# Optimization experiments

Measured on AMD Instinct MI355X. Metric: run time of the kernel, lower is better.

The kernel has to match this reference:

```python
import jax, jax.numpy as jnp
import numpy as np

B, S, PLM, G = 8, 2048, 768, 256
N_WM, E_WM = 50000, 800000
N_F, E_F = B * S, 131072
K = 4


def _gnn(h, src, dst, Ws, bs, n_nodes):
    # simple GCN-style message passing: aggregate neighbor features via
    # gather (h[src]) + scatter-add (segment_sum), then linear + relu.
    for W, b in zip(Ws, bs):
        m = jax.ops.segment_sum(h[src], dst, num_segments=n_nodes)  # [n, g]
        h = jax.nn.relu((h + m) @ W + b)
    return h


def setup_inputs() -> dict:
    key = jax.random.key(0)
    ks = jax.random.split(key, 16)
    std = 0.02
    inp = {
        "text_embeddings": jax.random.normal(ks[0], (B, S, PLM), jnp.float32),
        "wm_x": jax.random.normal(ks[1], (N_WM, G), jnp.float32),
        "wm_edge_index": jax.random.randint(ks[2], (2, E_WM), 0, N_WM),
        "token2nodepos": jax.random.randint(ks[3], (B * S, K), 0, N_WM),
        "fstm_node_ids": jax.random.randint(ks[4], (N_F,), 0, N_F),
        "fstm_edge_index": jax.random.randint(ks[5], (2, E_F), 0, N_F),
        # extra_emb: nn.Embedding(2, G, padding_idx=0) -> row 0 is zeros
        "extra_emb": jax.random.normal(ks[6], (2, G), jnp.float32).at[0].set(0.0) * std,
        "wm_W1": jax.random.normal(ks[7], (G, G), jnp.float32) * std,
        "wm_b1": jnp.zeros((G,), jnp.float32),
        "wm_W2": jax.random.normal(ks[8], (G, G), jnp.float32) * std,
        "wm_b2": jnp.zeros((G,), jnp.float32),
        "fstm_W1": jax.random.normal(ks[9], (G, G), jnp.float32) * std,
        "fstm_b1": jnp.zeros((G,), jnp.float32),
        "fstm_W2": jax.random.normal(ks[10], (G, G), jnp.float32) * std,
        "fstm_b2": jnp.zeros((G,), jnp.float32),
        "fc1_W": jax.random.normal(ks[11], (G + PLM, G), jnp.float32) * std,
        "fc1_b": jnp.zeros((G,), jnp.float32),
        "fc3_W": jax.random.normal(ks[12], (PLM + 2 * G, PLM), jnp.float32) * std,
        "fc3_b": jnp.zeros((PLM,), jnp.float32),
    }
    return inp


def reference(text_embeddings, wm_x, wm_edge_index, token2nodepos, fstm_node_ids,
              fstm_edge_index, extra_emb, wm_W1, wm_b1, wm_W2, wm_b2,
              fstm_W1, fstm_b1, fstm_W2, fstm_b2, fc1_W, fc1_b, fc3_W, fc3_b):
    # ====== WM ======
    graph_embeddings = _gnn(wm_x, wm_edge_index[0], wm_edge_index[1],
                            (wm_W1, wm_W2), (wm_b1, wm_b2), N_WM)  # [N_WM, G]
    table = jnp.concatenate([extra_emb, graph_embeddings], axis=0)  # [N_WM+2, G]
    # per-token gather-sum over K concept slots (original python loop, vectorized)
    tmp = jnp.sum(table[token2nodepos + 2], axis=1)  # [B*S, G]
    text_flat = text_embeddings.reshape(B * S, PLM)
    graph_text_embed = jnp.concatenate([tmp, text_flat], axis=-1) @ fc1_W + fc1_b  # [B*S, G]
    # ====== FSTM ======
    x = graph_text_embed[fstm_node_ids]  # [B*S, G]
    temporal = _gnn(x, fstm_edge_index[0], fstm_edge_index[1],
                    (fstm_W1, fstm_W2), (fstm_b1, fstm_b2), N_F)
    temporal = temporal.reshape(B, S, G)
    # ====== Final ======
    final_vec = jnp.concatenate(
        [text_embeddings, tmp.reshape(B, S, G), temporal], axis=-1)
    logits = final_vec @ fc3_W + fc3_b  # [B, S, PLM]
    return logits
```

## Files before the change

kernel.cpp:

```cpp
#include <hip/hip_runtime.h>

#define Bsz 8
#define Ssz 2048
#define PLM 768
#define Gd  256
#define N_WM 50000
#define E_WM 800000
#define N_F  16384
#define E_F  131072
#define Kc   4

typedef unsigned short ushort_t;
typedef short short8 __attribute__((ext_vector_type(8)));
typedef float f32x4 __attribute__((ext_vector_type(4)));

__device__ __forceinline__ ushort_t f2bf(float f) {
    union { float f; unsigned int u; } v; v.f = f;
    unsigned int r = (v.u + 0x7fffu + ((v.u >> 16) & 1u)) >> 16;
    return (ushort_t)r;
}
__device__ __forceinline__ float bf2f(ushort_t b) {
    union { unsigned int u; float f; } v; v.u = ((unsigned int)b) << 16;
    return v.f;
}
__device__ __forceinline__ float4 bf4f(ushort4 u) {
    return make_float4(bf2f(u.x), bf2f(u.y), bf2f(u.z), bf2f(u.w));
}

__device__ __forceinline__ void gl2lds16(const ushort_t* g, ushort_t* l) {
    __builtin_amdgcn_global_load_lds(
        (const __attribute__((address_space(1))) unsigned int*)g,
        (__attribute__((address_space(3))) unsigned int*)l, 16, 0, 0);
}

__device__ __forceinline__ void cvt4(const float* __restrict__ in,
                                     ushort_t* __restrict__ out, int i, int n4) {
    if (i < n4) {
        float4 v = ((const float4*)in)[i];
        ushort4 u;
        u.x = f2bf(v.x); u.y = f2bf(v.y); u.z = f2bf(v.z); u.w = f2bf(v.w);
        ((ushort4*)out)[i] = u;
    }
}

__device__ __forceinline__ void wtx_tile(const float* __restrict__ W,
                                         ushort_t* __restrict__ Wt,
                                         int K, int N, int tile,
                                         ushort_t (*sm)[65]) {
    int kt = K >> 6;
    int k0 = (tile % kt) << 6;
    int n0 = (tile / kt) << 6;
    int t = threadIdx.x;
    int tr = t >> 6, tc = t & 63;
#pragma unroll
    for (int p = 0; p < 16; ++p) {
        int k = p * 4 + tr;
        sm[k][tc] = f2bf(W[(size_t)(k0 + k) * N + n0 + tc]);
    }
    __syncthreads();
#pragma unroll
    for (int p = 0; p < 16; ++p) {
        int n = p * 4 + tr;
        Wt[(size_t)(n0 + n) * K + k0 + tc] = sm[tc][n];
    }
}

__global__ void conv_all(const float* __restrict__ wm_x, const float* __restrict__ text,
                         const float* __restrict__ extra,
                         const float* __restrict__ W1, const float* __restrict__ W2,
                         const float* __restrict__ W3, const float* __restrict__ W4,
                         const float* __restrict__ W5, const float* __restrict__ W6,
                         ushort_t* __restrict__ Xb, ushort_t* __restrict__ Tx,
                         ushort_t* __restrict__ Exb,
                         ushort_t* __restrict__ T1, ushort_t* __restrict__ T2,
                         ushort_t* __restrict__ T3, ushort_t* __restrict__ T4,
                         ushort_t* __restrict__ T5, ushort_t* __restrict__ T6) {
    __shared__ ushort_t sm[64][65];
    int b = blockIdx.x, t = threadIdx.x;
    if (b < 12500) { cvt4(wm_x, Xb, b * 256 + t, 3200000); return; }
    b -= 12500;
    if (b < 12288) { cvt4(text, Tx, b * 256 + t, 3145728); return; }
    b -= 12288;
    if (b < 1) { cvt4(extra, Exb, t, 128); return; }
    b -= 1;
    if (b < 16) { wtx_tile(W1, T1, 256, 256, b, sm); return; }
    b -= 16;
    if (b < 16) { wtx_tile(W2, T2, 256, 256, b, sm); return; }
    b -= 16;
    if (b < 16) { wtx_tile(W3, T3, 256, 256, b, sm); return; }
    b -= 16;
    if (b < 16) { wtx_tile(W4, T4, 256, 256, b, sm); return; }
    b -= 16;
    if (b < 64) { wtx_tile(W5, T5, 1024, 256, b, sm); return; }
    b -= 64;
    wtx_tile(W6, T6, 1280, 768, b, sm);
}

#define WM_P 512
#define WM_CH 1563
#define WM_SHIFT 8
#define FS_P 128
#define FS_CH 1024
#define FS_SHIFT 6

__global__ __launch_bounds__(256) void csr_p1(const int* __restrict__ wm_dst,
                                              const int* __restrict__ f_dst,
                                              int* __restrict__ Cwm,
                                              int* __restrict__ Cfs) {
    __shared__ int hist[256];
    int b = blockIdx.x, t = threadIdx.x;
    hist[t] = 0; __syncthreads();
    if (b < WM_P) {
        int e0 = b * WM_CH, e1 = e0 + WM_CH; if (e1 > E_WM) e1 = E_WM;
        for (int e = e0 + t; e < e1; e += 256)
            atomicAdd(&hist[wm_dst[e] >> WM_SHIFT], 1);
        __syncthreads();
        Cwm[b * 256 + t] = hist[t];
    } else {
        int p = b - WM_P;
        int e0 = p * FS_CH, e1 = e0 + FS_CH;
        for (int e = e0 + t; e < e1; e += 256)
            atomicAdd(&hist[f_dst[e] >> FS_SHIFT], 1);
        __syncthreads();
        Cfs[p * 256 + t] = hist[t];
    }
}

__global__ __launch_bounds__(256) void csr_p2a(int* __restrict__ Cwm, int* __restrict__ BTwm,
                                               int* __restrict__ Cfs, int* __restrict__ BTfs) {
    __shared__ int sm[256];
    int b = blockIdx.x, t = threadIdx.x;
    int* C; int* BT; int P; int bk;
    if (b < 256) { C = Cwm; BT = BTwm; P = WM_P; bk = b; }
    else         { C = Cfs; BT = BTfs; P = FS_P; bk = b - 256; }
    int half = P >> 1;
    int v0 = 0, v1 = 0;
    if (t < half) { v0 = C[(2 * t) * 256 + bk]; v1 = C[(2 * t + 1) * 256 + bk]; }
    int s = v0 + v1;
    sm[t] = s; __syncthreads();
#pragma unroll
    for (int st = 1; st < 256; st <<= 1) {
        int x = (t >= st) ? sm[t - st] : 0;
        __syncthreads();
        sm[t] += x;
        __syncthreads();
    }
    int ex = sm[t] - s;
    if (t < half) {
        C[(2 * t) * 256 + bk] = ex;
        C[(2 * t + 1) * 256 + bk] = ex + v0;
    }
    if (t == 255) BT[bk] = sm[255];
}

__global__ __launch_bounds__(256) void csr_p2b(const int* __restrict__ BTwm,
                                               int* __restrict__ BSwm,
                                               const int* __restrict__ BTfs,
                                               int* __restrict__ BSfs) {
    __shared__ int sm[256];
    int t = threadIdx.x;
    const int* BT = blockIdx.x ? BTfs : BTwm;
    int* BS = blockIdx.x ? BSfs : BSwm;
    int E = blockIdx.x ? E_F : E_WM;
    int v = BT[t];
    sm[t] = v; __syncthreads();
#pragma unroll
    for (int st = 1; st < 256; st <<= 1) {
        int x = (t >= st) ? sm[t - st] : 0;
        __syncthreads();
        sm[t] += x;
        __syncthreads();
    }
    BS[t] = sm[t] - v;
    if (t == 255) BS[256] = E;
}

__global__ __launch_bounds__(256) void csr_p3(const int* __restrict__ wm_src,
                                              const int* __restrict__ wm_dst,
                                              const int* __restrict__ Cwm,
                                              const int* __restrict__ BSwm,
                                              int2* __restrict__ SEwm,
                                              const int* __restrict__ f_src,
                                              const int* __restrict__ f_dst,
                                              const int* __restrict__ Cfs,
                                              const int* __restrict__ BSfs,
                                              int2* __restrict__ SEfs) {
    __shared__ int cur[256];
    int b = blockIdx.x, t = threadIdx.x;
    if (b < WM_P) {
        cur[t] = Cwm[b * 256 + t] + BSwm[t];
        __syncthreads();
        int e0 = b * WM_CH, e1 = e0 + WM_CH; if (e1 > E_WM) e1 = E_WM;
        for (int e = e0 + t; e < e1; e += 256) {
            int d = wm_dst[e], s = wm_src[e];
            int pos = atomicAdd(&cur[d >> WM_SHIFT], 1);
            SEwm[pos] = make_int2(s, d);
        }
    } else {
        int p = b - WM_P;
        cur[t] = Cfs[p * 256 + t] + BSfs[t];
        __syncthreads();
        int e0 = p * FS_CH, e1 = e0 + FS_CH;
        for (int e = e0 + t; e < e1; e += 256) {
            int d = f_dst[e], s = f_src[e];
            int pos = atomicAdd(&cur[d >> FS_SHIFT], 1);
            SEfs[pos] = make_int2(s, d);
        }
    }
}

__global__ __launch_bounds__(256) void csr_p4(const int2* __restrict__ SEwm,
                                              const int* __restrict__ BSwm,
                                              int* __restrict__ wm_off,
                                              int* __restrict__ wm_bkt,
                                              const int2* __restrict__ SEfs,
                                              const int* __restrict__ BSfs,
                                              int* __restrict__ fs_off,
                                              int* __restrict__ fs_bkt) {
    __shared__ int cnt[256];
    __shared__ int sm[256];
    int ob = blockIdx.x, t = threadIdx.x;
    const int2* SE; const int* BS; int* off; int* bkt;
    int b, nb0, n, E, bw;
    if (ob < 256) { SE = SEwm; BS = BSwm; off = wm_off; bkt = wm_bkt;
                    b = ob; nb0 = b << WM_SHIFT; n = N_WM; E = E_WM; bw = 256; }
    else          { SE = SEfs; BS = BSfs; off = fs_off; bkt = fs_bkt;
                    b = ob - 256; nb0 = b << FS_SHIFT; n = N_F; E = E_F; bw = 64; }
    int e0 = BS[b], e1 = BS[b + 1];
    cnt[t] = 0; __syncthreads();
    for (int e = e0 + t; e < e1; e += 256)
        atomicAdd(&cnt[SE[e].y - nb0], 1);
    __syncthreads();
    int v = cnt[t];
    sm[t] = v; __syncthreads();
#pragma unroll
    for (int st = 1; st < 256; st <<= 1) {
        int x = (t >= st) ? sm[t - st] : 0;
        __syncthreads();
        sm[t] += x;
        __syncthreads();
    }
    int ex = sm[t] - v;
    if (t < bw && nb0 + t < n) off[nb0 + t] = e0 + ex;
    if (b == 0 && t == 0) off[n] = E;
    __syncthreads();
    cnt[t] = e0 + ex;
    __syncthreads();
    for (int e = e0 + t; e < e1; e += 256) {
        int2 sd = SE[e];
        int pos = atomicAdd(&cnt[sd.y - nb0], 1);
        bkt[pos] = sd.x;
    }
}

__global__ void aggregate_kernel(const ushort_t* __restrict__ h,
                                 const int* __restrict__ off,
                                 const int* __restrict__ bucket,
                                 ushort_t* __restrict__ hm, int n) {
    int i = blockIdx.x * 4 + (threadIdx.x >> 6);
    if (i >= n) return;
    int lane = threadIdx.x & 63;
    int s0 = off[i], s1 = off[i + 1];
    const ushort4* hp = (const ushort4*)h;
    float4 acc = bf4f(hp[(size_t)i * 64 + lane]);
    int j = s0;
    for (; j + 16 <= s1; j += 16) {
        int bb[16];
#pragma unroll
        for (int q = 0; q < 16; ++q) bb[q] = bucket[j + q];
        ushort4 rr[16];
#pragma unroll
        for (int q = 0; q < 16; ++q) rr[q] = hp[(size_t)bb[q] * 64 + lane];
#pragma unroll
        for (int q = 0; q < 16; ++q) {
            float4 v = bf4f(rr[q]);
            acc.x += v.x; acc.y += v.y; acc.z += v.z; acc.w += v.w;
        }
    }
    for (; j + 4 <= s1; j += 4) {
        int bb[4];
#pragma unroll
        for (int q = 0; q < 4; ++q) bb[q] = bucket[j + q];
        ushort4 rr[4];
#pragma unroll
        for (int q = 0; q < 4; ++q) rr[q] = hp[(size_t)bb[q] * 64 + lane];
#pragma unroll
        for (int q = 0; q < 4; ++q) {
            float4 v = bf4f(rr[q]);
            acc.x += v.x; acc.y += v.y; acc.z += v.z; acc.w += v.w;
        }
    }
    for (; j < s1; ++j) {
        float4 v = bf4f(hp[(size_t)bucket[j] * 64 + lane]);
        acc.x += v.x; acc.y += v.y; acc.z += v.z; acc.w += v.w;
    }
    ushort4 u;
    u.x = f2bf(acc.x); u.y = f2bf(acc.y); u.z = f2bf(acc.z); u.w = f2bf(acc.w);
    ((ushort4*)hm)[(size_t)i * 64 + lane] = u;
}

__global__ void tmp_kernel(const ushort_t* __restrict__ gemb,
                           const ushort_t* __restrict__ extra,
                           const int* __restrict__ t2np,
                           ushort_t* __restrict__ D) {
    int i = blockIdx.x * 4 + (threadIdx.x >> 6);
    int lane = threadIdx.x & 63;
    float4 s = make_float4(0.f, 0.f, 0.f, 0.f);
#pragma unroll
    for (int k = 0; k < Kc; ++k) {
        int idx = t2np[i * Kc + k] + 2;
        const ushort4* row = (idx < 2) ? (const ushort4*)(extra + (size_t)idx * Gd)
                                       : (const ushort4*)(gemb + (size_t)(idx - 2) * Gd);
        float4 v = bf4f(row[lane]);
        s.x += v.x; s.y += v.y; s.z += v.z; s.w += v.w;
    }
    ushort4 u;
    u.x = f2bf(s.x); u.y = f2bf(s.y); u.z = f2bf(s.z); u.w = f2bf(s.w);
    ((ushort4*)D)[(size_t)i * 64 + lane] = u;
}

__global__ void gather_kernel(const ushort_t* __restrict__ Ein,
                              const int* __restrict__ ids,
                              ushort_t* __restrict__ F) {
    int i = blockIdx.x * 4 + (threadIdx.x >> 6);
    int lane = threadIdx.x & 63;
    ((ushort4*)F)[(size_t)i * 64 + lane] =
        ((const ushort4*)Ein)[(size_t)ids[i] * 64 + lane];
}

#define TBK 64
#define GBM 64
#define GBN 128

__device__ __forceinline__ void xcd_swizzle(int& bx, int& by) {
    int gx = gridDim.x;
    int nwg = gx * gridDim.y;
    int orig = by * gx + bx;
    int q = nwg >> 3, r = nwg & 7;
    int xcd = orig & 7, loc = orig >> 3;
    int wg = (xcd < r ? xcd * (q + 1) : r * (q + 1) + (xcd - r) * q) + loc;
    bx = wg % gx;
    by = wg / gx;
}

template <int MODE, int OUTBF, int BM, int BN>
__global__ __launch_bounds__(256) void mfma_gemm(
    const ushort_t* __restrict__ p0, const ushort_t* __restrict__ p1,
    const ushort_t* __restrict__ p2, const ushort_t* __restrict__ Wt,
    const float* __restrict__ bias, void* __restrict__ Cv,
    int M, int N, int K, int relu) {
    constexpr int MR = BM / 32;
    constexpr int NR = BN / 32;
    constexpr int A_IT = (BM * TBK) / 2048;
    constexpr int B_IT = (BN * TBK) / 2048;
    __shared__ ushort_t As[BM * TBK];
    __shared__ ushort_t Bs[BN * TBK];

    int tid  = threadIdx.x;
    int lane = tid & 63;
    int wave = tid >> 6;
    int wm = (wave >> 1) * (BM / 2), wn = (wave & 1) * (BN / 2);
    int bx = blockIdx.x, by = blockIdx.y;
    xcd_swizzle(bx, by);
    int row0 = by * BM, col0 = bx * BN;
    int l15 = lane & 15, l4 = lane >> 4;

    f32x4 acc[MR][NR];
#pragma unroll
    for (int i = 0; i < MR; ++i)
#pragma unroll
        for (int j = 0; j < NR; ++j)
            acc[i][j] = (f32x4){0.f, 0.f, 0.f, 0.f};

    for (int k0 = 0; k0 < K; k0 += TBK) {
#pragma unroll
        for (int it = 0; it < A_IT; ++it) {
            int eb = it * 2048 + wave * 512;
            int le = eb + lane * 8;
            int r  = le >> 6;
            int kl = (le ^ ((r & 7) << 3)) & 63;
            int grow = row0 + r; if (grow > M - 1) grow = M - 1;
            int gk = k0 + kl;
            const ushort_t* gp;
            if (MODE == 0)
                gp = p0 + (size_t)grow * K + gk;
            else if (MODE == 2)
                gp = (gk < 256) ? p0 + (size_t)grow * 256 + gk
                                : p1 + (size_t)grow * 768 + (gk - 256);
            else
                gp = (gk < 768) ? p0 + (size_t)grow * 768 + gk
                   : (gk < 1024) ? p1 + (size_t)grow * 256 + (gk - 768)
                                 : p2 + (size_t)grow * 256 + (gk - 1024);
            gl2lds16(gp, &As[eb]);
        }
#pragma unroll
        for (int it = 0; it < B_IT; ++it) {
            int eb = it * 2048 + wave * 512;
            int le = eb + lane * 8;
            int nl = le >> 6;
            int kl = (le ^ ((nl & 7) << 3)) & 63;
            const ushort_t* gp = Wt + (size_t)(col0 + nl) * K + k0 + kl;
            gl2lds16(gp, &Bs[eb]);
        }
        __syncthreads();

#pragma unroll
        for (int ks = 0; ks < TBK; ks += 32) {
            short8 af[MR], bfr[NR];
#pragma unroll
            for (int mi = 0; mi < MR; ++mi) {
                int row = wm + mi * 16 + l15;
                int col = (ks + l4 * 8) ^ ((row & 7) << 3);
                af[mi] = *(const short8*)&As[row * TBK + col];
            }
#pragma unroll
            for (int ni = 0; ni < NR; ++ni) {
                int row = wn + ni * 16 + l15;
                int col = (ks + l4 * 8) ^ ((row & 7) << 3);
                bfr[ni] = *(const short8*)&Bs[row * TBK + col];
            }
#pragma unroll
            for (int mi = 0; mi < MR; ++mi)
#pragma unroll
                for (int ni = 0; ni < NR; ++ni)
                    acc[mi][ni] = __builtin_amdgcn_mfma_f32_16x16x32_bf16(
                        af[mi], bfr[ni], acc[mi][ni], 0, 0, 0);
        }
        __syncthreads();
    }

#pragma unroll
    for (int ni = 0; ni < NR; ++ni) {
        int c = col0 + wn + ni * 16 + l15;
        float bv = bias[c];
#pragma unroll
        for (int mi = 0; mi < MR; ++mi) {
#pragma unroll
            for (int r = 0; r < 4; ++r) {
                int rr = row0 + wm + mi * 16 + l4 * 4 + r;
                if (rr < M) {
                    float v = acc[mi][ni][r] + bv;
                    if (relu) v = fmaxf(v, 0.f);
                    if (OUTBF) ((ushort_t*)Cv)[(size_t)rr * N + c] = f2bf(v);
                    else       ((float*)Cv)[(size_t)rr * N + c] = v;
                }
            }
        }
    }
}

extern "C" void kernel_launch(void* const* d_in, const int* in_sizes, int n_in,
                              void* d_out, int out_size, void* d_ws, size_t ws_size,
                              hipStream_t stream) {
    const float* text    = (const float*)d_in[0];
    const float* wm_x    = (const float*)d_in[1];
    const int*   wm_ei   = (const int*)d_in[2];
    const int*   t2np    = (const int*)d_in[3];
    const int*   f_ids   = (const int*)d_in[4];
    const int*   f_ei    = (const int*)d_in[5];
    const float* extra   = (const float*)d_in[6];
    const float* wm_W1   = (const float*)d_in[7];
    const float* wm_b1   = (const float*)d_in[8];
    const float* wm_W2   = (const float*)d_in[9];
    const float* wm_b2   = (const float*)d_in[10];
    const float* fs_W1   = (const float*)d_in[11];
    const float* fs_b1   = (const float*)d_in[12];
    const float* fs_W2   = (const float*)d_in[13];
    const float* fs_b2   = (const float*)d_in[14];
    const float* fc1_W   = (const float*)d_in[15];
    const float* fc1_b   = (const float*)d_in[16];
    const float* fc3_W   = (const float*)d_in[17];
    const float* fc3_b   = (const float*)d_in[18];
    float* out = (float*)d_out;

    ushort_t* Xb  = (ushort_t*)d_ws;
    ushort_t* Ag  = Xb + 12800000;
    ushort_t* Gm  = Ag + 12800000;
    ushort_t* Tx  = Gm + 12800000;
    ushort_t* Dt  = Tx + 12582912;
    ushort_t* Ee  = Dt + 4194304;
    ushort_t* Wv  = Ee + 4194304;
    ushort_t* wt_wm1 = Wv;
    ushort_t* wt_wm2 = wt_wm1 + 65536;
    ushort_t* wt_fs1 = wt_wm2 + 65536;
    ushort_t* wt_fs2 = wt_fs1 + 65536;
    ushort_t* wt_fc1 = wt_fs2 + 65536;
    ushort_t* wt_fc3 = wt_fc1 + 262144;
    ushort_t* Exb    = wt_fc3 + 983040;
    int* wm_off = (int*)(Exb + 512);
    int* fs_off = wm_off + N_WM + 1;
    int* wm_bkt = fs_off + N_F + 1;
    int* fs_bkt = wm_bkt + E_WM;
    int2* SEwm = (int2*)Ag;
    int2* SEfs = SEwm + E_WM;
    int*  Cwm  = (int*)(SEfs + E_F);
    int*  Cfs  = Cwm + WM_P * 256;
    int*  BTwm = Cfs + FS_P * 256;
    int*  BTfs = BTwm + 256;
    int*  BSwm = BTfs + 256;
    int*  BSfs = BSwm + 257;

    ushort_t* h1 = Xb;
    ushort_t* F  = Gm;
    ushort_t* H  = Gm + 4194304;
    ushort_t* T  = Ee;

    const int* wm_src = wm_ei;
    const int* wm_dst = wm_ei + E_WM;
    const int* f_src  = f_ei;
    const int* f_dst  = f_ei + E_F;

    dim3 blk(256);
    dim3 gW(Gd / GBN, (N_WM + GBM - 1) / GBM);
    dim3 gF(Gd / GBN, N_F / GBM);
    dim3 gO(PLM / GBN, N_F / GBM);

    csr_p1<<<WM_P + FS_P, blk, 0, stream>>>(wm_dst, f_dst, Cwm, Cfs);
    csr_p2a<<<512, blk, 0, stream>>>(Cwm, BTwm, Cfs, BTfs);
    csr_p2b<<<2, blk, 0, stream>>>(BTwm, BSwm, BTfs, BSfs);
    csr_p3<<<WM_P + FS_P, blk, 0, stream>>>(wm_src, wm_dst, Cwm, BSwm, SEwm,
                                            f_src, f_dst, Cfs, BSfs, SEfs);
    csr_p4<<<512, blk, 0, stream>>>(SEwm, BSwm, wm_off, wm_bkt,
                                    SEfs, BSfs, fs_off, fs_bkt);

    conv_all<<<25157, blk, 0, stream>>>(wm_x, text, extra,
                                        wm_W1, wm_W2, fs_W1, fs_W2, fc1_W, fc3_W,
                                        Xb, Tx, Exb,
                                        wt_wm1, wt_wm2, wt_fs1, wt_fs2,
                                        wt_fc1, wt_fc3);

    aggregate_kernel<<<(N_WM + 3) / 4, blk, 0, stream>>>(Xb, wm_off, wm_bkt, Ag, N_WM);
    mfma_gemm<0, 1, GBM, GBN><<<gW, blk, 0, stream>>>(Ag, nullptr, nullptr, wt_wm1,
                                                      wm_b1, h1, N_WM, Gd, Gd, 1);
    aggregate_kernel<<<(N_WM + 3) / 4, blk, 0, stream>>>(h1, wm_off, wm_bkt, Ag, N_WM);
    mfma_gemm<0, 1, GBM, GBN><<<gW, blk, 0, stream>>>(Ag, nullptr, nullptr, wt_wm2,
                                                      wm_b2, Gm, N_WM, Gd, Gd, 1);
    tmp_kernel<<<N_F / 4, blk, 0, stream>>>(Gm, Exb, t2np, Dt);
    mfma_gemm<2, 1, GBM, GBN><<<gF, blk, 0, stream>>>(Dt, Tx, nullptr, wt_fc1,
                                                      fc1_b, Ee, N_F, Gd, Gd + PLM, 0);
    gather_kernel<<<N_F / 4, blk, 0, stream>>>(Ee, f_ids, F);
    aggregate_kernel<<<N_F / 4, blk, 0, stream>>>(F, fs_off, fs_bkt, Ag, N_F);
    mfma_gemm<0, 1, GBM, GBN><<<gF, blk, 0, stream>>>(Ag, nullptr, nullptr, wt_fs1,
                                                      fs_b1, H, N_F, Gd, Gd, 1);
    aggregate_kernel<<<N_F / 4, blk, 0, stream>>>(H, fs_off, fs_bkt, Ag, N_F);
    mfma_gemm<0, 1, GBM, GBN><<<gF, blk, 0, stream>>>(Ag, nullptr, nullptr, wt_fs2,
                                                      fs_b2, T, N_F, Gd, Gd, 1);
    mfma_gemm<3, 0, GBM, GBN><<<gO, blk, 0, stream>>>(Tx, Dt, T, wt_fc3, fc3_b,
                                                      out, N_F, PLM, PLM + 2 * Gd, 0);
}
```

Before: 533.5 us.

## Slice WM node features into feature-major chunks for cache-friendly aggregation

Stores WM node features in eight 32-column slices (slice-major layout), written that way by the input conversion and by the first WM GEMM epilogue. A new sliced aggregation kernel assigns each block one slice, so gathers hit a 3.2 MB per-slice working set that fits in cache better than full 512-byte rows. The GEMM gains a mode that reads this layout, and the remaining aggregation kernel's unroll drops from 16 to 8. The cost is narrower 4-byte gathers per lane, eight times as many index reads, and scattered epilogue stores.

```diff
diff --git a/kernel.cpp b/kernel.cpp
--- a/kernel.cpp
+++ b/kernel.cpp
@@ -11,6 +11,7 @@
 #define Kc   4
 
 typedef unsigned short ushort_t;
+typedef unsigned int uint_t;
 typedef short short8 __attribute__((ext_vector_type(8)));
 typedef float f32x4 __attribute__((ext_vector_type(4)));
 
@@ -32,6 +33,9 @@
         (const __attribute__((address_space(1))) unsigned int*)g,
         (__attribute__((address_space(3))) unsigned int*)l, 16, 0, 0);
 }
+
+#define NSL 8
+#define SLW 32
 
 __device__ __forceinline__ void cvt4(const float* __restrict__ in,
                                      ushort_t* __restrict__ out, int i, int n4) {
@@ -40,6 +44,20 @@
         ushort4 u;
         u.x = f2bf(v.x); u.y = f2bf(v.y); u.z = f2bf(v.z); u.w = f2bf(v.w);
         ((ushort4*)out)[i] = u;
+    }
+}
+
+__device__ __forceinline__ void cvt4_sm(const float* __restrict__ in,
+                                        ushort_t* __restrict__ out, int i, int n4,
+                                        int nrows) {
+    if (i < n4) {
+        float4 v = ((const float4*)in)[i];
+        int flat = i * 4;
+        int node = flat >> 8, c = flat & 255;
+        int s = c >> 5, cc = c & 31;
+        ushort4 u;
+        u.x = f2bf(v.x); u.y = f2bf(v.y); u.z = f2bf(v.z); u.w = f2bf(v.w);
+        *(ushort4*)&out[((size_t)s * nrows + node) * SLW + cc] = u;
     }
 }
 
@@ -77,7 +95,7 @@
                          ushort_t* __restrict__ T5, ushort_t* __restrict__ T6) {
     __shared__ ushort_t sm[64][65];
     int b = blockIdx.x, t = threadIdx.x;
-    if (b < 12500) { cvt4(wm_x, Xb, b * 256 + t, 3200000); return; }
+    if (b < 12500) { cvt4_sm(wm_x, Xb, b * 256 + t, 3200000, N_WM); return; }
     b -= 12500;
     if (b < 12288) { cvt4(text, Tx, b * 256 + t, 3145728); return; }
     b -= 12288;
@@ -253,6 +271,43 @@
     }
 }
 
+__global__ __launch_bounds__(256) void aggregate_sliced(
+        const ushort_t* __restrict__ h, const int* __restrict__ off,
+        const int* __restrict__ bucket, ushort_t* __restrict__ hm, int n) {
+    int bid = blockIdx.x;
+    int s = bid & 7, nb = bid >> 3;
+    int t = threadIdx.x;
+    int g = t >> 4, li = t & 15;
+    int i = nb * 16 + g;
+    if (i >= n) return;
+    const uint_t* hp = (const uint_t*)(h + (size_t)s * n * SLW);
+    uint_t* op = (uint_t*)(hm + (size_t)s * n * SLW);
+    int s0 = off[i], s1 = off[i + 1];
+    uint_t dv = hp[i * 16 + li];
+    float ax = bf2f((ushort_t)(dv & 0xffffu));
+    float ay = bf2f((ushort_t)(dv >> 16));
+    int j = s0;
+    for (; j + 8 <= s1; j += 8) {
+        int bb[8];
+#pragma unroll
+        for (int q = 0; q < 8; ++q) bb[q] = bucket[j + q];
+        uint_t rr[8];
+#pragma unroll
+        for (int q = 0; q < 8; ++q) rr[q] = hp[bb[q] * 16 + li];
+#pragma unroll
+        for (int q = 0; q < 8; ++q) {
+            ax += bf2f((ushort_t)(rr[q] & 0xffffu));
+            ay += bf2f((ushort_t)(rr[q] >> 16));
+        }
+    }
+    for (; j < s1; ++j) {
+        uint_t r = hp[bucket[j] * 16 + li];
+        ax += bf2f((ushort_t)(r & 0xffffu));
+        ay += bf2f((ushort_t)(r >> 16));
+    }
+    op[i * 16 + li] = ((uint_t)f2bf(ay) << 16) | (uint_t)f2bf(ax);
+}
+
 __global__ void aggregate_kernel(const ushort_t* __restrict__ h,
                                  const int* __restrict__ off,
                                  const int* __restrict__ bucket,
@@ -264,28 +319,15 @@
     const ushort4* hp = (const ushort4*)h;
     float4 acc = bf4f(hp[(size_t)i * 64 + lane]);
     int j = s0;
-    for (; j + 16 <= s1; j += 16) {
-        int bb[16];
-#pragma unroll
-        for (int q = 0; q < 16; ++q) bb[q] = bucket[j + q];
-        ushort4 rr[16];
-#pragma unroll
-        for (int q = 0; q < 16; ++q) rr[q] = hp[(size_t)bb[q] * 64 + lane];
-#pragma unroll
-        for (int q = 0; q < 16; ++q) {
-            float4 v = bf4f(rr[q]);
-            acc.x += v.x; acc.y += v.y; acc.z += v.z; acc.w += v.w;
-        }
-    }
-    for (; j + 4 <= s1; j += 4) {
-        int bb[4];
-#pragma unroll
-        for (int q = 0; q < 4; ++q) bb[q] = bucket[j + q];
-        ushort4 rr[4];
-#pragma unroll
-        for (int q = 0; q < 4; ++q) rr[q] = hp[(size_t)bb[q] * 64 + lane];
-#pragma unroll
-        for (int q = 0; q < 4; ++q) {
+    for (; j + 8 <= s1; j += 8) {
+        int bb[8];
+#pragma unroll
+        for (int q = 0; q < 8; ++q) bb[q] = bucket[j + q];
+        ushort4 rr[8];
+#pragma unroll
+        for (int q = 0; q < 8; ++q) rr[q] = hp[(size_t)bb[q] * 64 + lane];
+#pragma unroll
+        for (int q = 0; q < 8; ++q) {
             float4 v = bf4f(rr[q]);
             acc.x += v.x; acc.y += v.y; acc.z += v.z; acc.w += v.w;
         }
@@ -343,7 +385,7 @@
     by = wg / gx;
 }
 
-template <int MODE, int OUTBF, int BM, int BN>
+template <int MODE, int OUTBF, int OUTSM, int BM, int BN>
 __global__ __launch_bounds__(256) void mfma_gemm(
     const ushort_t* __restrict__ p0, const ushort_t* __restrict__ p1,
     const ushort_t* __restrict__ p2, const ushort_t* __restrict__ Wt,
@@ -384,6 +426,8 @@
             const ushort_t* gp;
             if (MODE == 0)
                 gp = p0 + (size_t)grow * K + gk;
+            else if (MODE == 1)
+                gp = p0 + ((size_t)(gk >> 5) * M + grow) * SLW + (gk & 31);
             else if (MODE == 2)
                 gp = (gk < 256) ? p0 + (size_t)grow * 256 + gk
                                 : p1 + (size_t)grow * 768 + (gk - 256);
@@ -441,8 +485,14 @@
                 if (rr < M) {
                     float v = acc[mi][ni][r] + bv;
                     if (relu) v = fmaxf(v, 0.f);
-                    if (OUTBF) ((ushort_t*)Cv)[(size_t)rr * N + c] = f2bf(v);
-                    else       ((float*)Cv)[(size_t)rr * N + c] = v;
+                    if (OUTBF) {
+                        if (OUTSM)
+                            ((ushort_t*)Cv)[((size_t)(c >> 5) * M + rr) * SLW + (c & 31)] = f2bf(v);
+                        else
+                            ((ushort_t*)Cv)[(size_t)rr * N + c] = f2bf(v);
+                    } else {
+                        ((float*)Cv)[(size_t)rr * N + c] = v;
+                    }
                 }
             }
         }
@@ -514,6 +564,7 @@
     dim3 gW(Gd / GBN, (N_WM + GBM - 1) / GBM);
     dim3 gF(Gd / GBN, N_F / GBM);
     dim3 gO(PLM / GBN, N_F / GBM);
+    const int gAggW = NSL * ((N_WM + 15) / 16);
 
     csr_p1<<<WM_P + FS_P, blk, 0, stream>>>(wm_dst, f_dst, Cwm, Cfs);
     csr_p2a<<<512, blk, 0, stream>>>(Cwm, BTwm, Cfs, BTfs);
@@ -529,22 +580,22 @@
                                         wt_wm1, wt_wm2, wt_fs1, wt_fs2,
                                         wt_fc1, wt_fc3);
 
-    aggregate_kernel<<<(N_WM + 3) / 4, blk, 0, stream>>>(Xb, wm_off, wm_bkt, Ag, N_WM);
-    mfma_gemm<0, 1, GBM, GBN><<<gW, blk, 0, stream>>>(Ag, nullptr, nullptr, wt_wm1,
-                                                      wm_b1, h1, N_WM, Gd, Gd, 1);
-    aggregate_kernel<<<(N_WM + 3) / 4, blk, 0, stream>>>(h1, wm_off, wm_bkt, Ag, N_WM);
-    mfma_gemm<0, 1, GBM, GBN><<<gW, blk, 0, stream>>>(Ag, nullptr, nullptr, wt_wm2,
-                                                      wm_b2, Gm, N_WM, Gd, Gd, 1);
+    aggregate_sliced<<<gAggW, blk, 0, stream>>>(Xb, wm_off, wm_bkt, Ag, N_WM);
+    mfma_gemm<1, 1, 1, GBM, GBN><<<gW, blk, 0, stream>>>(Ag, nullptr, nullptr, wt_wm1,
+                                                         wm_b1, h1, N_WM, Gd, Gd, 1);
+    aggregate_sliced<<<gAggW, blk, 0, stream>>>(h1, wm_off, wm_bkt, Ag, N_WM);
+    mfma_gemm<1, 1, 0, GBM, GBN><<<gW, blk, 0, stream>>>(Ag, nullptr, nullptr, wt_wm2,
+                                                         wm_b2, Gm, N_WM, Gd, Gd, 1);
     tmp_kernel<<<N_F / 4, blk, 0, stream>>>(Gm, Exb, t2np, Dt);
-    mfma_gemm<2, 1, GBM, GBN><<<gF, blk, 0, stream>>>(Dt, Tx, nullptr, wt_fc1,
-                                                      fc1_b, Ee, N_F, Gd, Gd + PLM, 0);
+    mfma_gemm<2, 1, 0, GBM, GBN><<<gF, blk, 0, stream>>>(Dt, Tx, nullptr, wt_fc1,
+                                                         fc1_b, Ee, N_F, Gd, Gd + PLM, 0);
     gather_kernel<<<N_F / 4, blk, 0, stream>>>(Ee, f_ids, F);
     aggregate_kernel<<<N_F / 4, blk, 0, stream>>>(F, fs_off, fs_bkt, Ag, N_F);
-    mfma_gemm<0, 1, GBM, GBN><<<gF, blk, 0, stream>>>(Ag, nullptr, nullptr, wt_fs1,
-                                                      fs_b1, H, N_F, Gd, Gd, 1);
+    mfma_gemm<0, 1, 0, GBM, GBN><<<gF, blk, 0, stream>>>(Ag, nullptr, nullptr, wt_fs1,
+                                                         fs_b1, H, N_F, Gd, Gd, 1);
     aggregate_kernel<<<N_F / 4, blk, 0, stream>>>(H, fs_off, fs_bkt, Ag, N_F);
-    mfma_gemm<0, 1, GBM, GBN><<<gF, blk, 0, stream>>>(Ag, nullptr, nullptr, wt_fs2,
-                                                      fs_b2, T, N_F, Gd, Gd, 1);
-    mfma_gemm<3, 0, GBM, GBN><<<gO, blk, 0, stream>>>(Tx, Dt, T, wt_fc3, fc3_b,
-                                                      out, N_F, PLM, PLM + 2 * Gd, 0);
-}
+    mfma_gemm<0, 1, 0, GBM, GBN><<<gF, blk, 0, stream>>>(Ag, nullptr, nullptr, wt_fs2,
+                                                         fs_b2, T, N_F, Gd, Gd, 1);
+    mfma_gemm<3, 0, 0, GBM, GBN><<<gO, blk, 0, stream>>>(Tx, Dt, T, wt_fc3, fc3_b,
+                                                         out, N_F, PLM, PLM + 2 * Gd, 0);
+}
```

New measurement: 543.2 us. Within noise of the previous version (+1.8%).

## Fuse neighbor aggregation with GNN linear layer and fold id gather into it

Applied to the files above, without the earlier changes.

Replaces the separate aggregate and GEMM kernels for each GNN layer with one kernel: each 512-thread block aggregates 64 node rows into shared memory in bf16 and then runs MFMA against the full 256-wide weight, writing bias+relu output. The FSTM input gather is folded in by indirecting through fstm_node_ids inside the aggregation, removing the gather kernel and its intermediate buffer. This removes intermediate global round trips and launches. In exchange, the B tile is reloaded per block, there are fewer waves per row for latency hiding, and the unroll depth drops from 16 to 8.

```diff
diff --git a/kernel.cpp b/kernel.cpp
--- a/kernel.cpp
+++ b/kernel.cpp
@@ -253,50 +253,120 @@
     }
 }
 
-__global__ void aggregate_kernel(const ushort_t* __restrict__ h,
-                                 const int* __restrict__ off,
-                                 const int* __restrict__ bucket,
-                                 ushort_t* __restrict__ hm, int n) {
-    int i = blockIdx.x * 4 + (threadIdx.x >> 6);
-    if (i >= n) return;
-    int lane = threadIdx.x & 63;
-    int s0 = off[i], s1 = off[i + 1];
+template <int IDS>
+__global__ __launch_bounds__(512) void fused_gnn(
+        const ushort_t* __restrict__ h, const int* __restrict__ ids,
+        const int* __restrict__ off, const int* __restrict__ bucket,
+        const ushort_t* __restrict__ Wt, const float* __restrict__ bias,
+        ushort_t* __restrict__ outp, int n, int relu) {
+    __shared__ ushort_t As[64 * 256];
+    __shared__ ushort_t Bs[256 * 64];
+    int tid = threadIdx.x;
+    int wave = tid >> 6, lane = tid & 63;
+    int r0 = blockIdx.x * 64;
+
     const ushort4* hp = (const ushort4*)h;
-    float4 acc = bf4f(hp[(size_t)i * 64 + lane]);
-    int j = s0;
-    for (; j + 16 <= s1; j += 16) {
-        int bb[16];
-#pragma unroll
-        for (int q = 0; q < 16; ++q) bb[q] = bucket[j + q];
-        ushort4 rr[16];
-#pragma unroll
-        for (int q = 0; q < 16; ++q) rr[q] = hp[(size_t)bb[q] * 64 + lane];
-#pragma unroll
-        for (int q = 0; q < 16; ++q) {
-            float4 v = bf4f(rr[q]);
+#pragma unroll 1
+    for (int rr = 0; rr < 8; ++rr) {
+        int lr = wave * 8 + rr;
+        int i = r0 + lr;
+        if (i > n - 1) i = n - 1;
+        int s0 = off[i], s1 = off[i + 1];
+        int self = IDS ? ids[i] : i;
+        float4 acc = bf4f(hp[(size_t)self * 64 + lane]);
+        int j = s0;
+        for (; j + 8 <= s1; j += 8) {
+            int bb[8];
+#pragma unroll
+            for (int q = 0; q < 8; ++q) {
+                int sx = bucket[j + q];
+                bb[q] = IDS ? ids[sx] : sx;
+            }
+            ushort4 rv[8];
+#pragma unroll
+            for (int q = 0; q < 8; ++q) rv[q] = hp[(size_t)bb[q] * 64 + lane];
+#pragma unroll
+            for (int q = 0; q < 8; ++q) {
+                float4 v = bf4f(rv[q]);
+                acc.x += v.x; acc.y += v.y; acc.z += v.z; acc.w += v.w;
+            }
+        }
+        for (; j < s1; ++j) {
+            int sx = bucket[j];
+            int b0 = IDS ? ids[sx] : sx;
+            float4 v = bf4f(hp[(size_t)b0 * 64 + lane]);
             acc.x += v.x; acc.y += v.y; acc.z += v.z; acc.w += v.w;
         }
-    }
-    for (; j + 4 <= s1; j += 4) {
-        int bb[4];
-#pragma unroll
-        for (int q = 0; q < 4; ++q) bb[q] = bucket[j + q];
-        ushort4 rr[4];
-#pragma unroll
-        for (int q = 0; q < 4; ++q) rr[q] = hp[(size_t)bb[q] * 64 + lane];
-#pragma unroll
-        for (int q = 0; q < 4; ++q) {
-            float4 v = bf4f(rr[q]);
-            acc.x += v.x; acc.y += v.y; acc.z += v.z; acc.w += v.w;
-        }
-    }
-    for (; j < s1; ++j) {
-        float4 v = bf4f(hp[(size_t)bucket[j] * 64 + lane]);
-        acc.x += v.x; acc.y += v.y; acc.z += v.z; acc.w += v.w;
-    }
-    ushort4 u;
-    u.x = f2bf(acc.x); u.y = f2bf(acc.y); u.z = f2bf(acc.z); u.w = f2bf(acc.w);
-    ((ushort4*)hm)[(size_t)i * 64 + lane] = u;
+        int c = lane * 4;
+        int cs = c ^ ((lr & 7) << 3);
+        ushort4 u;
+        u.x = f2bf(acc.x); u.y = f2bf(acc.y); u.z = f2bf(acc.z); u.w = f2bf(acc.w);
+        *(ushort4*)&As[lr * 256 + cs] = u;
+    }
+    __syncthreads();
+
+    int wm = (wave >> 2) * 32, wn = (wave & 3) * 64;
+    int l15 = lane & 15, l4 = lane >> 4;
+    f32x4 acc[2][4];
+#pragma unroll
+    for (int mi = 0; mi < 2; ++mi)
+#pragma unroll
+        for (int ni = 0; ni < 4; ++ni)
+            acc[mi][ni] = (f32x4){0.f, 0.f, 0.f, 0.f};
+
+    for (int k0 = 0; k0 < 256; k0 += 64) {
+#pragma unroll
+        for (int it = 0; it < 4; ++it) {
+            int eb = it * 4096 + wave * 512;
+            int le = eb + lane * 8;
+            int nl = le >> 6;
+            int kl = (le ^ ((nl & 7) << 3)) & 63;
+            const ushort_t* gp = Wt + (size_t)nl * 256 + k0 + kl;
+            gl2lds16(gp, &Bs[eb]);
+        }
+        __syncthreads();
+#pragma unroll
+        for (int ks = 0; ks < 64; ks += 32) {
+            short8 af[2], bfr[4];
+#pragma unroll
+            for (int mi = 0; mi < 2; ++mi) {
+                int row = wm + mi * 16 + l15;
+                int col = (k0 + ks + l4 * 8) ^ ((row & 7) << 3);
+                af[mi] = *(const short8*)&As[row * 256 + col];
+            }
+#pragma unroll
+            for (int ni = 0; ni < 4; ++ni) {
+                int cb = wn + ni * 16 + l15;
+                int ck = (ks + l4 * 8) ^ ((cb & 7) << 3);
+                bfr[ni] = *(const short8*)&Bs[cb * 64 + ck];
+            }
+#pragma unroll
+            for (int mi = 0; mi < 2; ++mi)
+#pragma unroll
+                for (int ni = 0; ni < 4; ++ni)
+                    acc[mi][ni] = __builtin_amdgcn_mfma_f32_16x16x32_bf16(
+                        af[mi], bfr[ni], acc[mi][ni], 0, 0, 0);
+        }
+        __syncthreads();
+    }
+
+#pragma unroll
+    for (int ni = 0; ni < 4; ++ni) {
+        int c = wn + ni * 16 + l15;
+        float bv = bias[c];
+#pragma unroll
+        for (int mi = 0; mi < 2; ++mi) {
+#pragma unroll
+            for (int r = 0; r < 4; ++r) {
+                int rr = r0 + wm + mi * 16 + l4 * 4 + r;
+                if (rr < n) {
+                    float v = acc[mi][ni][r] + bv;
+                    if (relu) v = fmaxf(v, 0.f);
+                    outp[(size_t)rr * 256 + c] = f2bf(v);
+                }
+            }
+        }
+    }
 }
 
 __global__ void tmp_kernel(const ushort_t* __restrict__ gemb,
@@ -317,15 +387,6 @@
     ushort4 u;
     u.x = f2bf(s.x); u.y = f2bf(s.y); u.z = f2bf(s.z); u.w = f2bf(s.w);
     ((ushort4*)D)[(size_t)i * 64 + lane] = u;
-}
-
-__global__ void gather_kernel(const ushort_t* __restrict__ Ein,
-                              const int* __restrict__ ids,
-                              ushort_t* __restrict__ F) {
-    int i = blockIdx.x * 4 + (threadIdx.x >> 6);
-    int lane = threadIdx.x & 63;
-    ((ushort4*)F)[(size_t)i * 64 + lane] =
-        ((const ushort4*)Ein)[(size_t)ids[i] * 64 + lane];
 }
 
 #define TBK 64
@@ -382,9 +443,7 @@
             int grow = row0 + r; if (grow > M - 1) grow = M - 1;
             int gk = k0 + kl;
             const ushort_t* gp;
-            if (MODE == 0)
-                gp = p0 + (size_t)grow * K + gk;
-            else if (MODE == 2)
+            if (MODE == 2)
                 gp = (gk < 256) ? p0 + (size_t)grow * 256 + gk
                                 : p1 + (size_t)grow * 768 + (gk - 256);
             else
@@ -500,8 +559,7 @@
     int*  BSwm = BTfs + 256;
     int*  BSfs = BSwm + 257;
 
-    ushort_t* h1 = Xb;
-    ushort_t* F  = Gm;
+    ushort_t* h1 = Ag;
     ushort_t* H  = Gm + 4194304;
     ushort_t* T  = Ee;
 
@@ -511,9 +569,11 @@
     const int* f_dst  = f_ei + E_F;
 
     dim3 blk(256);
-    dim3 gW(Gd / GBN, (N_WM + GBM - 1) / GBM);
+    dim3 blk512(512);
     dim3 gF(Gd / GBN, N_F / GBM);
     dim3 gO(PLM / GBN, N_F / GBM);
+    const int gWM = (N_WM + 63) / 64;
+    const int gFS = N_F / 64;
 
     csr_p1<<<WM_P + FS_P, blk, 0, stream>>>(wm_dst, f_dst, Cwm, Cfs);
     csr_p2a<<<512, blk, 0, stream>>>(Cwm, BTwm, Cfs, BTfs);
@@ -529,22 +589,17 @@
                                         wt_wm1, wt_wm2, wt_fs1, wt_fs2,
                                         wt_fc1, wt_fc3);
 
-    aggregate_kernel<<<(N_WM + 3) / 4, blk, 0, stream>>>(Xb, wm_off, wm_bkt, Ag, N_WM);
-    mfma_gemm<0, 1, GBM, GBN><<<gW, blk, 0, stream>>>(Ag, nullptr, nullptr, wt_wm1,
-                                                      wm_b1, h1, N_WM, Gd, Gd, 1);
-    aggregate_kernel<<<(N_WM + 3) / 4, blk, 0, stream>>>(h1, wm_off, wm_bkt, Ag, N_WM);
-    mfma_gemm<0, 1, GBM, GBN><<<gW, blk, 0, stream>>>(Ag, nullptr, nullptr, wt_wm2,
-                                                      wm_b2, Gm, N_WM, Gd, Gd, 1);
+    fused_gnn<0><<<gWM, blk512, 0, stream>>>(Xb, nullptr, wm_off, wm_bkt,
+                                             wt_wm1, wm_b1, h1, N_WM, 1);
+    fused_gnn<0><<<gWM, blk512, 0, stream>>>(h1, nullptr, wm_off, wm_bkt,
+                                             wt_wm2, wm_b2, Gm, N_WM, 1);
     tmp_kernel<<<N_F / 4, blk, 0, stream>>>(Gm, Exb, t2np, Dt);
     mfma_gemm<2, 1, GBM, GBN><<<gF, blk, 0, stream>>>(Dt, Tx, nullptr, wt_fc1,
                                                       fc1_b, Ee, N_F, Gd, Gd + PLM, 0);
-    gather_kernel<<<N_F / 4, blk, 0, stream>>>(Ee, f_ids, F);
-    aggregate_kernel<<<N_F / 4, blk, 0, stream>>>(F, fs_off, fs_bkt, Ag, N_F);
-    mfma_gemm<0, 1, GBM, GBN><<<gF, blk, 0, stream>>>(Ag, nullptr, nullptr, wt_fs1,
-                                                      fs_b1, H, N_F, Gd, Gd, 1);
-    aggregate_kernel<<<N_F / 4, blk, 0, stream>>>(H, fs_off, fs_bkt, Ag, N_F);
-    mfma_gemm<0, 1, GBM, GBN><<<gF, blk, 0, stream>>>(Ag, nullptr, nullptr, wt_fs2,
-                                                      fs_b2, T, N_F, Gd, Gd, 1);
+    fused_gnn<1><<<gFS, blk512, 0, stream>>>(Ee, f_ids, fs_off, fs_bkt,
+                                             wt_fs1, fs_b1, H, N_F, 1);
+    fused_gnn<0><<<gFS, blk512, 0, stream>>>(H, nullptr, fs_off, fs_bkt,
+                                             wt_fs2, fs_b2, T, N_F, 1);
     mfma_gemm<3, 0, GBM, GBN><<<gO, blk, 0, stream>>>(Tx, Dt, T, wt_fc3, fc3_b,
                                                       out, N_F, PLM, PLM + 2 * Gd, 0);
 }
```

New measurement: 569.3 us. +6.7%, slower.
